# Kernel optimization log

Hardware: AMD Instinct MI355X
Metric: run time of the kernel (lower is better)

Reference implementation:

```python
import jax, jax.numpy as jnp
import numpy as np

B, T, H, V, S = 32, 1024, 512, 1024, 128
PAD = 0          # PAD_token, also the CTC blank
NEG = -1e30      # finite stand-in for -inf (grad-safe)


def setup_inputs() -> dict:
    key = jax.random.key(0)
    ks = jax.random.split(key, 5)
    padded_input = jax.random.normal(ks[0], (B, T, H), dtype=jnp.float32)
    # labels in [1, V) so no PAD inside targets -> target_lengths == S
    padded_target = jax.random.randint(ks[1], (B, S), 1, V).astype(jnp.int32)
    input_lengths = jax.random.randint(ks[2], (B,), T // 2, T + 1).astype(jnp.int32)
    W1 = jax.random.normal(ks[3], (H, H), dtype=jnp.float32) * 0.02
    b1 = jnp.zeros((H,), jnp.float32)
    W2 = jax.random.normal(ks[4], (H, V), dtype=jnp.float32) * 0.02
    b2 = jnp.zeros((V,), jnp.float32)
    return {"padded_target": padded_target, "padded_input": padded_input,
            "input_lengths": input_lengths, "W1": W1, "b1": b1, "W2": W2, "b2": b2}


def _ctc_loss(log_probs, targets, input_lengths, target_lengths, blank=PAD):
    """CTC negative log-likelihood per example (reduction='none').
    log_probs: [B,T,V] (log-softmaxed), targets: [B,S] int."""
    Bb, Tt, _ = log_probs.shape
    Ss = targets.shape[1]
    L = 2 * Ss + 1  # extended label sequence: blank,y1,blank,...,yS,blank
    ext = jnp.full((Bb, L), blank, dtype=targets.dtype).at[:, 1::2].set(targets)
    # gather log-probs of extended labels: [B,T,L] -> [T,B,L]
    lp_ext = jnp.take_along_axis(
        log_probs, jnp.broadcast_to(ext[:, None, :], (Bb, Tt, L)), axis=2)
    lp_ext = jnp.transpose(lp_ext, (1, 0, 2))
    # skip transition (s-2 -> s) allowed when ext[s] != blank and ext[s] != ext[s-2]
    skip = jnp.concatenate(
        [jnp.zeros((Bb, 2), bool),
         (ext[:, 2:] != blank) & (ext[:, 2:] != ext[:, :-2])], axis=1)

    alpha0 = jnp.full((Bb, L), NEG, jnp.float32)
    alpha0 = alpha0.at[:, 0].set(lp_ext[0, :, 0]).at[:, 1].set(lp_ext[0, :, 1])

    def step(alpha, xs):
        lp_t, t = xs
        s1 = jnp.concatenate([jnp.full((Bb, 1), NEG, jnp.float32), alpha[:, :-1]], axis=1)
        s2 = jnp.concatenate([jnp.full((Bb, 2), NEG, jnp.float32), alpha[:, :-2]], axis=1)
        a = jnp.logaddexp(alpha, s1)
        a = jnp.where(skip, jnp.logaddexp(a, s2), a)
        new = a + lp_t
        # freeze alpha past each example's input length
        new = jnp.where((t < input_lengths)[:, None], new, alpha)
        return new, None

    alpha, _ = jax.lax.scan(step, alpha0, (lp_ext[1:], jnp.arange(1, Tt)))
    end1 = jnp.take_along_axis(alpha, (2 * target_lengths - 1)[:, None], axis=1)[:, 0]
    end2 = jnp.take_along_axis(alpha, (2 * target_lengths)[:, None], axis=1)[:, 0]
    return -jnp.logaddexp(end1, end2)


def reference(padded_target, padded_input, input_lengths, W1, b1, W2, b2):
    target_lengths = jnp.sum(padded_target != PAD, axis=1).astype(jnp.int32)
    h = jnp.tanh(padded_input @ W1 + b1)          # [B,T,H]
    logits = h @ W2 + b2                           # [B,T,V]
    log_probs = jax.nn.log_softmax(logits, axis=-1)
    loss = _ctc_loss(log_probs, padded_target, input_lengths, target_lengths)
    return loss / target_lengths.astype(jnp.float32)  # [B]
```

## Files before the change

### kernel.cpp

```cpp
#include <hip/hip_runtime.h>
#include <hip/hip_bf16.h>
#include <math.h>

#define Bq 32
#define Tt 1024
#define Hh 512
#define Vv 1024
#define Ss 128

typedef short bf16x8 __attribute__((ext_vector_type(8)));
typedef float f32x4 __attribute__((ext_vector_type(4)));

#define GLDS(srcp, dstp, sz) \
  __builtin_amdgcn_global_load_lds( \
      (const __attribute__((address_space(1))) void*)(srcp), \
      (__attribute__((address_space(3))) void*)(dstp), sz, 0, 0)

__device__ __forceinline__ ushort f2bf(float v) {
  __hip_bfloat16 hv = __float2bfloat16(v);
  return *(ushort*)&hv;
}

#define BFLY_MAX(v) { \
  v = fmaxf(v, __int_as_float(__builtin_amdgcn_ds_swizzle(__float_as_int(v), 0x041F))); \
  v = fmaxf(v, __int_as_float(__builtin_amdgcn_ds_swizzle(__float_as_int(v), 0x081F))); \
  v = fmaxf(v, __int_as_float(__builtin_amdgcn_ds_swizzle(__float_as_int(v), 0x101F))); \
  v = fmaxf(v, __int_as_float(__builtin_amdgcn_ds_swizzle(__float_as_int(v), 0x201F))); }
#define BFLY_ADD(v) { \
  v += __int_as_float(__builtin_amdgcn_ds_swizzle(__float_as_int(v), 0x041F)); \
  v += __int_as_float(__builtin_amdgcn_ds_swizzle(__float_as_int(v), 0x081F)); \
  v += __int_as_float(__builtin_amdgcn_ds_swizzle(__float_as_int(v), 0x101F)); \
  v += __int_as_float(__builtin_amdgcn_ds_swizzle(__float_as_int(v), 0x201F)); }

__global__ void transpose_cvt(const float* __restrict__ in, ushort* __restrict__ out,
                              int K, int N) {
  __shared__ float tile[32][33];
  const int k0 = blockIdx.y * 32, n0 = blockIdx.x * 32;
  const int tx = threadIdx.x, ty = threadIdx.y;
  for (int i = ty; i < 32; i += 8)
    tile[i][tx] = in[(size_t)(k0 + i) * N + n0 + tx];
  __syncthreads();
  for (int i = ty; i < 32; i += 8)
    out[(size_t)(n0 + i) * K + k0 + tx] = f2bf(tile[tx][i]);
}

__global__ __launch_bounds__(256, 2)
void gemm1_fused(const float* __restrict__ A, const ushort* __restrict__ Bt,
                 const float* __restrict__ bias, ushort* __restrict__ H) {
  __shared__ ushort As[2][128 * 64];
  __shared__ ushort Bs[2][128 * 64];
  const int tid = threadIdx.x;
  const int lane = tid & 63, wave = tid >> 6;
  const int wm = wave >> 1, wn = wave & 1;
  const int q = lane >> 4, r16 = lane & 15;
  const int row0 = blockIdx.y * 128, col0 = blockIdx.x * 128;
  const int lrow = lane >> 3;
  const int swz = (lane & 7) ^ lrow;
  const int ra_ = tid >> 3;
  const int ca_ = tid & 7;
  const int ga_ = ca_ ^ (ra_ & 7);
  const int rx = r16 & 7;
  const int kx0 = (q ^ rx) * 8;
  const int kx1 = ((4 + q) ^ rx) * 8;

  float4 rA[4][2];
  auto loadA = [&](int kk) {
#pragma unroll
    for (int p = 0; p < 4; ++p) {
      const float* src = A + (size_t)(row0 + p * 32 + ra_) * Hh + kk * 64 + ga_ * 8;
      rA[p][0] = *(const float4*)(src);
      rA[p][1] = *(const float4*)(src + 4);
    }
  };
  auto storeA = [&](int d) {
#pragma unroll
    for (int p = 0; p < 4; ++p) {
      unsigned w0 = ((unsigned)f2bf(rA[p][0].y) << 16) | f2bf(rA[p][0].x);
      unsigned w1 = ((unsigned)f2bf(rA[p][0].w) << 16) | f2bf(rA[p][0].z);
      unsigned w2 = ((unsigned)f2bf(rA[p][1].y) << 16) | f2bf(rA[p][1].x);
      unsigned w3 = ((unsigned)f2bf(rA[p][1].w) << 16) | f2bf(rA[p][1].z);
      uint4 u = {w0, w1, w2, w3};
      *(uint4*)&As[d][(p * 32 + ra_) * 64 + ca_ * 8] = u;
    }
  };
  auto stageB = [&](int kk, int d) {
#pragma unroll
    for (int i = 0; i < 4; ++i) {
      const int seg = wave * 4 + i;
      const int rr = seg * 8 + lrow;
      GLDS(Bt + (size_t)(col0 + rr) * Hh + kk * 64 + swz * 8, &Bs[d][seg * 512], 16);
    }
  };

  f32x4 acc[4][4];
#pragma unroll
  for (int i = 0; i < 4; ++i)
#pragma unroll
    for (int j = 0; j < 4; ++j) acc[i][j] = (f32x4){0.f, 0.f, 0.f, 0.f};

  loadA(0);
  stageB(0, 0);
  storeA(0);
  loadA(1);
  __syncthreads();

  for (int kk = 0; kk < 8; ++kk) {
    const int d = kk & 1;
    if (kk < 7) { stageB(kk + 1, d ^ 1); storeA(d ^ 1); }
    if (kk < 6) loadA(kk + 2);
#pragma unroll
    for (int ksl = 0; ksl < 2; ++ksl) {
      const int kxo = ksl ? kx1 : kx0;
      bf16x8 af[4], bfr[4];
#pragma unroll
      for (int mi = 0; mi < 4; ++mi)
        af[mi] = *(const bf16x8*)(&As[d][((wm * 64 + mi * 16 + r16) << 6) + kxo]);
#pragma unroll
      for (int ni = 0; ni < 4; ++ni)
        bfr[ni] = *(const bf16x8*)(&Bs[d][((wn * 64 + ni * 16 + r16) << 6) + kxo]);
#pragma unroll
      for (int mi = 0; mi < 4; ++mi)
#pragma unroll
        for (int ni = 0; ni < 4; ++ni)
          acc[mi][ni] = __builtin_amdgcn_mfma_f32_16x16x32_bf16(af[mi], bfr[ni], acc[mi][ni], 0, 0, 0);
    }
    __syncthreads();
  }

#pragma unroll
  for (int ni = 0; ni < 4; ++ni) {
    const int col = col0 + wn * 64 + ni * 16 + r16;
    const float bc = bias[col];
#pragma unroll
    for (int mi = 0; mi < 4; ++mi) {
#pragma unroll
      for (int r = 0; r < 4; ++r) {
        const int row = row0 + wm * 64 + mi * 16 + q * 4 + r;
        const float v = acc[mi][ni][r] + bc;
        const float ex = __expf(2.0f * v);
        const float rc = 1.0f / (ex + 1.0f);
        H[(size_t)row * Hh + col] = f2bf((ex - 1.0f) * rc);
      }
    }
  }
}

__global__ __launch_bounds__(256, 2)
void gemm2sm(const ushort* __restrict__ Aq, const ushort* __restrict__ Bt,
             const float* __restrict__ bias, const int* __restrict__ tgt,
             ushort* __restrict__ pOdd, ushort* __restrict__ pBlank) {
  __shared__ ushort Bs[2][128 * 64];
  __shared__ float biasLds[Vv];
  __shared__ int tgLds[128];
  __shared__ float rowM[64], rowS[64], sfArr[64], blankL[64];
  __shared__ float tmpM[2][64], tmpS[2][64];

  const int tid = threadIdx.x;
  const int lane = tid & 63, wave = tid >> 6;
  const int wm = wave >> 1, wn = wave & 1;
  const int q = lane >> 4, r16 = lane & 15;
  const int row0 = blockIdx.x * 64;
  const int bEx = blockIdx.x >> 4;
  const int lrow = lane >> 3;
  const int swz = (lane & 7) ^ lrow;
  const int rx = r16 & 7;
  const int kx0 = (q ^ rx) * 8;
  const int kx1 = ((4 + q) ^ rx) * 8;

  GLDS(bias + tid * 4, (char*)biasLds + wave * 1024, 16);
  if (tid < 128) tgLds[tid] = tgt[bEx * Ss + tid];
  if (tid < 64) { rowM[tid] = -1e30f; rowS[tid] = 0.f; }

  bf16x8 af[16][2];
#pragma unroll
  for (int ks = 0; ks < 16; ++ks)
#pragma unroll
    for (int mi = 0; mi < 2; ++mi)
      af[ks][mi] = *(const bf16x8*)(Aq + (size_t)(row0 + wm * 32 + mi * 16 + r16) * Hh + ks * 32 + q * 8);

  auto stageB = [&](int nt, int kk, int d) {
#pragma unroll
    for (int i = 0; i < 4; ++i) {
      const int seg = wave * 4 + i;
      const int rr = seg * 8 + lrow;
      const int kko = kk * 64 + swz * 8;
      const ushort* src;
      if (nt < 8) src = Bt + (size_t)(nt * 128 + rr) * Hh + kko;
      else        src = Bt + (size_t)tgLds[rr] * Hh + kko;
      GLDS(src, &Bs[d][seg * 512], 16);
    }
  };

  stageB(0, 0, 0);

  f32x4 acc[2][4];
#pragma unroll
  for (int i = 0; i < 2; ++i)
#pragma unroll
    for (int j = 0; j < 4; ++j) acc[i][j] = (f32x4){0.f, 0.f, 0.f, 0.f};

  for (int nt = 0; nt < 9; ++nt) {
#pragma unroll
    for (int kk = 0; kk < 8; ++kk) {
      const int d = kk & 1;
      __syncthreads();
      if (!(nt == 8 && kk == 7)) {
        const int ntn = (kk < 7) ? nt : nt + 1;
        const int kkn = (kk < 7) ? kk + 1 : 0;
        stageB(ntn, kkn, d ^ 1);
      }
#pragma unroll
      for (int ksl = 0; ksl < 2; ++ksl) {
        const int kxo = ksl ? kx1 : kx0;
        bf16x8 bfr[4];
#pragma unroll
        for (int ni = 0; ni < 4; ++ni)
          bfr[ni] = *(const bf16x8*)(&Bs[d][((wn * 64 + ni * 16 + r16) << 6) + kxo]);
#pragma unroll
        for (int mi = 0; mi < 2; ++mi)
#pragma unroll
          for (int ni = 0; ni < 4; ++ni)
            acc[mi][ni] = __builtin_amdgcn_mfma_f32_16x16x32_bf16(af[kk * 2 + ksl][mi], bfr[ni], acc[mi][ni], 0, 0, 0);
      }
    }

    if (nt < 8) {
      float bcol[4];
#pragma unroll
      for (int ni = 0; ni < 4; ++ni) bcol[ni] = biasLds[nt * 128 + wn * 64 + ni * 16 + r16];

      float tm[2][4];
#pragma unroll
      for (int mi = 0; mi < 2; ++mi)
#pragma unroll
        for (int r = 0; r < 4; ++r) {
          float m = acc[mi][0][r] + bcol[0];
          m = fmaxf(m, acc[mi][1][r] + bcol[1]);
          m = fmaxf(m, acc[mi][2][r] + bcol[2]);
          m = fmaxf(m, acc[mi][3][r] + bcol[3]);
          BFLY_MAX(m);
          tm[mi][r] = m;
        }
      if (r16 == 0) {
#pragma unroll
        for (int mi = 0; mi < 2; ++mi) {
          float4 w = {tm[mi][0], tm[mi][1], tm[mi][2], tm[mi][3]};
          *(float4*)&tmpM[wn][wm * 32 + mi * 16 + q * 4] = w;
        }
        if (nt == 0 && wn == 0) {
#pragma unroll
          for (int mi = 0; mi < 2; ++mi) {
            float4 w = {acc[mi][0][0] + bcol[0], acc[mi][0][1] + bcol[0],
                        acc[mi][0][2] + bcol[0], acc[mi][0][3] + bcol[0]};
            *(float4*)&blankL[wm * 32 + mi * 16 + q * 4] = w;
          }
        }
      }
      __syncthreads();
      if (tid < 64) {
        const float old = rowM[tid];
        const float nm = fmaxf(old, fmaxf(tmpM[0][tid], tmpM[1][tid]));
        rowM[tid] = nm;
        sfArr[tid] = __expf(old - nm);
      }
      __syncthreads();
#pragma unroll
      for (int mi = 0; mi < 2; ++mi) {
        const float4 nm4 = *(const float4*)&rowM[wm * 32 + mi * 16 + q * 4];
#pragma unroll
        for (int r = 0; r < 4; ++r) {
          const float nm = ((const float*)&nm4)[r];
          float s = __expf(acc[mi][0][r] + bcol[0] - nm);
          s += __expf(acc[mi][1][r] + bcol[1] - nm);
          s += __expf(acc[mi][2][r] + bcol[2] - nm);
          s += __expf(acc[mi][3][r] + bcol[3] - nm);
          BFLY_ADD(s);
          tm[mi][r] = s;
        }
      }
      if (r16 == 0) {
#pragma unroll
        for (int mi = 0; mi < 2; ++mi) {
          float4 w = {tm[mi][0], tm[mi][1], tm[mi][2], tm[mi][3]};
          *(float4*)&tmpS[wn][wm * 32 + mi * 16 + q * 4] = w;
        }
      }
      __syncthreads();
      if (tid < 64)
        rowS[tid] = rowS[tid] * sfArr[tid] + tmpS[0][tid] + tmpS[1][tid];
#pragma unroll
      for (int i = 0; i < 2; ++i)
#pragma unroll
        for (int j = 0; j < 4; ++j) acc[i][j] = (f32x4){0.f, 0.f, 0.f, 0.f};
    } else {
      __syncthreads();
      if (tid < 64) {
        const float rc = rowM[tid] + __logf(rowS[tid]);
        sfArr[tid] = rc;
        pBlank[row0 + tid] = f2bf(__expf(blankL[tid] - rc) * 64.0f);
      }
      __syncthreads();
      float bcl[4];
#pragma unroll
      for (int ni = 0; ni < 4; ++ni) bcl[ni] = biasLds[tgLds[wn * 64 + ni * 16 + r16]];
#pragma unroll
      for (int mi = 0; mi < 2; ++mi) {
        const float4 rc4 = *(const float4*)&sfArr[wm * 32 + mi * 16 + q * 4];
#pragma unroll
        for (int r = 0; r < 4; ++r) {
          const float rc = ((const float*)&rc4)[r];
          const int row = row0 + wm * 32 + mi * 16 + q * 4 + r;
#pragma unroll
          for (int ni = 0; ni < 4; ++ni) {
            const float p = __expf(acc[mi][ni][r] + bcl[ni] - rc) * 64.0f;
            pOdd[(size_t)row * Ss + wn * 64 + ni * 16 + r16] = f2bf(p);
          }
        }
      }
    }
  }
}

__device__ __forceinline__ float dpp_wshr1(float x) {
  return __int_as_float(__builtin_amdgcn_update_dpp(
      0, __float_as_int(x), 0x138, 0xf, 0xf, true));
}
__device__ __forceinline__ float dpp_wave_max(float m) {
  m = fmaxf(m, __int_as_float(__builtin_amdgcn_update_dpp(0, __float_as_int(m), 0x111, 0xf, 0xf, true)));
  m = fmaxf(m, __int_as_float(__builtin_amdgcn_update_dpp(0, __float_as_int(m), 0x112, 0xf, 0xf, true)));
  m = fmaxf(m, __int_as_float(__builtin_amdgcn_update_dpp(0, __float_as_int(m), 0x114, 0xf, 0xf, true)));
  m = fmaxf(m, __int_as_float(__builtin_amdgcn_update_dpp(0, __float_as_int(m), 0x118, 0xf, 0xf, true)));
  m = fmaxf(m, __int_as_float(__builtin_amdgcn_update_dpp(__float_as_int(m), __float_as_int(m), 0x142, 0xf, 0xf, false)));
  m = fmaxf(m, __int_as_float(__builtin_amdgcn_update_dpp(__float_as_int(m), __float_as_int(m), 0x143, 0xf, 0xf, false)));
  return __int_as_float(__builtin_amdgcn_readlane(__float_as_int(m), 63));
}

__global__ __launch_bounds__(64)
void ctc_dp(const ushort* __restrict__ pOddG, const ushort* __restrict__ pBlankG,
            const int* __restrict__ tgt, const int* __restrict__ lens,
            float* __restrict__ out) {
  __shared__ ushort pO[2][72 * 128];
  __shared__ ushort pBl[2][128];
  const int b = blockIdx.x, l = threadIdx.x;
  const ushort* pObase = pOddG + (size_t)b * Tt * Ss;
  const ushort* pBbase = pBlankG + (size_t)b * Tt;
  const int* tg = tgt + b * Ss;
  const int len = lens[b];

  float sk1 = 0.f, sk3;
  if (l >= 1) sk1 = (tg[2 * l] != tg[2 * l - 1]) ? 1.f : 0.f;
  sk3 = (tg[2 * l + 1] != tg[2 * l]) ? 1.f : 0.f;

  auto stage = [&](int c, int d) {
    const ushort* src = pObase + (size_t)c * 64 * 128;
#pragma unroll
    for (int i = 0; i < 16; ++i)
      GLDS(src + (i * 64 + l) * 8, &pO[d][i * 512], 16);
    GLDS(pBbase + c * 64 + l * 2, &pBl[d][0], 4);
  };

  stage(0, 0);
  __syncthreads();

  float a0 = 0.f, a1 = 0.f, a2 = 0.f, a3 = 0.f, a4 = 0.f;
  if (l == 0) {
    a0 = __int_as_float(((unsigned)pBl[0][0]) << 16);
    a1 = __int_as_float(((unsigned)pO[0][0]) << 16);
  }
  int E = 0;

  auto renorm = [&]() {
    float m = fmaxf(fmaxf(fmaxf(a0, a1), fmaxf(a2, a3)), a4);
    const float gm = dpp_wave_max(m);
    const int e = (int)((__float_as_uint(gm) >> 23) & 255) - 127;
    int sh = 30 - e; if (sh > 120) sh = 120;
    const float scale = __uint_as_float((unsigned)(127 + sh) << 23);
    E -= sh;
    a0 *= scale; a1 *= scale; a2 *= scale; a3 *= scale; a4 *= scale;
  };

  auto run_dyn = [&](int d, int stA, int stB, int tbase) {
    const int n = stB - stA;
    if (n <= 0) return;
    unsigned qL[4], qB[4];
#pragma unroll
    for (int k = 0; k < 4; ++k) {
      const int st = stA + k;
      qL[k] = *(const unsigned*)&pO[d][(st << 7) + 2 * l];
      qB[k] = (unsigned)pBl[d][st];
    }
    auto body = [&](int i, int k) {
      const float pOa = __int_as_float(qL[k] << 16);
      const float pObv = __int_as_float(qL[k] & 0xffff0000u);
      const float pB = __int_as_float(qB[k] << 16);
      const float h3 = dpp_wshr1(a3);
      const float n0 = (a0 + h3) * pB;
      const float n1 = fmaf(sk1, h3, a1 + a0) * pOa;
      const float n2 = (a2 + a1) * pB;
      const float n3 = fmaf(sk3, a1, a3 + a2) * pObv;
      const float n4 = (a4 + a3) * pB;
      a0 = n0; a1 = n1; a2 = n2; a3 = n3; a4 = n4;
      const int st2 = stA + i + 4;
      qL[k] = *(const unsigned*)&pO[d][(st2 << 7) + 2 * l];
      qB[k] = (unsigned)pBl[d][st2];
      if (((tbase + i) & 7) == 0) renorm();
    };
    int i = 0;
    for (; i + 4 <= n; i += 4) { body(i, 0); body(i + 1, 1); body(i + 2, 2); body(i + 3, 3); }
    if ((n & 3) > 0) body(i, 0);
    if ((n & 3) > 1) body(i + 1, 1);
    if ((n & 3) > 2) body(i + 2, 2);
  };

  auto run_full = [&](int d) {
    unsigned qL[8], qB[4];
#pragma unroll
    for (int k = 0; k < 8; ++k)
      qL[k] = *(const unsigned*)&pO[d][(k << 7) + 2 * l];
#pragma unroll
    for (int j = 0; j < 4; ++j)
      qB[j] = *(const unsigned*)&pBl[d][2 * j];
    for (int i = 0; i < 64; i += 8) {
#pragma unroll
      for (int k = 0; k < 8; ++k) {
        const float pOa = __int_as_float(qL[k] << 16);
        const float pObv = __int_as_float(qL[k] & 0xffff0000u);
        const unsigned bb = qB[k >> 1];
        const float pB = __int_as_float((k & 1) ? (bb & 0xffff0000u) : (bb << 16));
        const float h3 = dpp_wshr1(a3);
        const float n0 = (a0 + h3) * pB;
        const float n1 = fmaf(sk1, h3, a1 + a0) * pOa;
        const float n2 = (a2 + a1) * pB;
        const float n3 = fmaf(sk3, a1, a3 + a2) * pObv;
        const float n4 = (a4 + a3) * pB;
        a0 = n0; a1 = n1; a2 = n2; a3 = n3; a4 = n4;
        qL[k] = *(const unsigned*)&pO[d][((i + k + 8) << 7) + 2 * l];
        if (k & 1) qB[k >> 1] = *(const unsigned*)&pBl[d][i + k + 7];
        if (k == 0) renorm();
      }
    }
  };

  if (64 < len) stage(1, 1);
  run_dyn(0, 1, (64 < len) ? 64 : len, 1);
  __syncthreads();
  const int Cfull = len >> 6;
  for (int c = 1; c < Cfull; ++c) {
    const int d = c & 1;
    if ((c + 1) * 64 < len) stage(c + 1, d ^ 1);
    run_full(d);
    __syncthreads();
  }
  if (len & 63) run_dyn(Cfull & 1, 0, len & 63, Cfull * 64);

  const int tl = __popcll(__ballot(tg[l] != 0)) + __popcll(__ballot(tg[64 + l] != 0));
  const int s1 = 2 * tl - 1, s2 = 2 * tl;
  float v = 0.f;
  const int sb = 4 * l;
  if (sb == s1 || sb == s2) v += a0;
  if (sb + 1 == s1 || sb + 1 == s2) v += a1;
  if (sb + 2 == s1 || sb + 2 == s2) v += a2;
  if (sb + 3 == s1 || sb + 3 == s2) v += a3;
  if (l == 63 && s2 == 256) v += a4;
#pragma unroll
  for (int off = 1; off < 64; off <<= 1) v += __shfl_xor(v, off);
  if (l == 0)
    out[b] = -((log2f(v) + (float)E - 6.0f * (float)len) * 0.6931471805599453f) / (float)tl;
}

extern "C" void kernel_launch(void* const* d_in, const int* in_sizes, int n_in,
                              void* d_out, int out_size, void* d_ws, size_t ws_size,
                              hipStream_t stream) {
  const int*   targets = (const int*)d_in[0];
  const float* X       = (const float*)d_in[1];
  const int*   lens    = (const int*)d_in[2];
  const float* W1      = (const float*)d_in[3];
  const float* b1      = (const float*)d_in[4];
  const float* W2      = (const float*)d_in[5];
  const float* b2      = (const float*)d_in[6];
  float* out = (float*)d_out;

  ushort* h       = (ushort*)d_ws;
  ushort* W1T     = h + (size_t)Bq * Tt * Hh;
  ushort* W2T     = W1T + (size_t)Hh * Hh;
  ushort* pOddG   = W2T + (size_t)Vv * Hh;
  ushort* pBlankG = pOddG + (size_t)Bq * Tt * Ss;

  transpose_cvt<<<dim3(Hh / 32, Hh / 32), dim3(32, 8), 0, stream>>>(W1, W1T, Hh, Hh);
  transpose_cvt<<<dim3(Vv / 32, Hh / 32), dim3(32, 8), 0, stream>>>(W2, W2T, Hh, Vv);
  gemm1_fused<<<dim3(Hh / 128, (Bq * Tt) / 128), dim3(256), 0, stream>>>(X, W1T, b1, h);
  gemm2sm<<<dim3((Bq * Tt) / 64), dim3(256), 0, stream>>>(h, W2T, b2, targets, pOddG, pBlankG);
  ctc_dp<<<dim3(Bq), dim3(64), 0, stream>>>(pOddG, pBlankG, targets, lens, out);
}
```

Before: 271.6 us.

## Restructure both GEMMs with register-resident A, triple-buffered B, and max-free softmax

gemm1 is rewritten so each block owns 64 rows of X. It converts them to bf16 once into registers and streams all four 128-column W1T tiles through a 3-stage LDS ring, using vmcnt-based waits instead of full barriers. gemm2 switches to the same 3-deep flat pipeline. Its online-softmax max tracking and per-tile barriers are replaced by a plain running sum of exp(logit), reduced once at the end. This removes per-tile cross-wave syncs, but it drops the max subtraction, so it relies on small logits to avoid overflow, and gemm1 now reloads W1T for every 64-row block.

```diff
diff --git a/kernel.cpp b/kernel.cpp
--- a/kernel.cpp
+++ b/kernel.cpp
@@ -21,11 +21,12 @@
   return *(ushort*)&hv;
 }
 
-#define BFLY_MAX(v) { \
-  v = fmaxf(v, __int_as_float(__builtin_amdgcn_ds_swizzle(__float_as_int(v), 0x041F))); \
-  v = fmaxf(v, __int_as_float(__builtin_amdgcn_ds_swizzle(__float_as_int(v), 0x081F))); \
-  v = fmaxf(v, __int_as_float(__builtin_amdgcn_ds_swizzle(__float_as_int(v), 0x101F))); \
-  v = fmaxf(v, __int_as_float(__builtin_amdgcn_ds_swizzle(__float_as_int(v), 0x201F))); }
+template <int N>
+__device__ __forceinline__ void wb() {
+  __asm__ volatile("s_waitcnt vmcnt(%0)" ::"i"(N) : "memory");
+  __builtin_amdgcn_s_barrier();
+}
+
 #define BFLY_ADD(v) { \
   v += __int_as_float(__builtin_amdgcn_ds_swizzle(__float_as_int(v), 0x041F)); \
   v += __int_as_float(__builtin_amdgcn_ds_swizzle(__float_as_int(v), 0x081F)); \
@@ -45,102 +46,94 @@
 }
 
 __global__ __launch_bounds__(256, 2)
-void gemm1_fused(const float* __restrict__ A, const ushort* __restrict__ Bt,
+void gemm1_fused(const float* __restrict__ X, const ushort* __restrict__ Bt,
                  const float* __restrict__ bias, ushort* __restrict__ H) {
-  __shared__ ushort As[2][128 * 64];
-  __shared__ ushort Bs[2][128 * 64];
+  __shared__ ushort Bs[3][128 * 64];
   const int tid = threadIdx.x;
   const int lane = tid & 63, wave = tid >> 6;
   const int wm = wave >> 1, wn = wave & 1;
   const int q = lane >> 4, r16 = lane & 15;
-  const int row0 = blockIdx.y * 128, col0 = blockIdx.x * 128;
+  const int row0 = blockIdx.x * 64;
   const int lrow = lane >> 3;
   const int swz = (lane & 7) ^ lrow;
-  const int ra_ = tid >> 3;
-  const int ca_ = tid & 7;
-  const int ga_ = ca_ ^ (ra_ & 7);
   const int rx = r16 & 7;
   const int kx0 = (q ^ rx) * 8;
   const int kx1 = ((4 + q) ^ rx) * 8;
 
-  float4 rA[4][2];
-  auto loadA = [&](int kk) {
-#pragma unroll
-    for (int p = 0; p < 4; ++p) {
-      const float* src = A + (size_t)(row0 + p * 32 + ra_) * Hh + kk * 64 + ga_ * 8;
-      rA[p][0] = *(const float4*)(src);
-      rA[p][1] = *(const float4*)(src + 4);
-    }
-  };
-  auto storeA = [&](int d) {
-#pragma unroll
-    for (int p = 0; p < 4; ++p) {
-      unsigned w0 = ((unsigned)f2bf(rA[p][0].y) << 16) | f2bf(rA[p][0].x);
-      unsigned w1 = ((unsigned)f2bf(rA[p][0].w) << 16) | f2bf(rA[p][0].z);
-      unsigned w2 = ((unsigned)f2bf(rA[p][1].y) << 16) | f2bf(rA[p][1].x);
-      unsigned w3 = ((unsigned)f2bf(rA[p][1].w) << 16) | f2bf(rA[p][1].z);
-      uint4 u = {w0, w1, w2, w3};
-      *(uint4*)&As[d][(p * 32 + ra_) * 64 + ca_ * 8] = u;
-    }
-  };
-  auto stageB = [&](int kk, int d) {
+  float bcolAll[4][4];
+#pragma unroll
+  for (int nt = 0; nt < 4; ++nt)
+#pragma unroll
+    for (int ni = 0; ni < 4; ++ni)
+      bcolAll[nt][ni] = bias[nt * 128 + wn * 64 + ni * 16 + r16];
+
+  bf16x8 af[16][2];
+#pragma unroll
+  for (int ks = 0; ks < 16; ++ks)
+#pragma unroll
+    for (int mi = 0; mi < 2; ++mi) {
+      const float* src = X + (size_t)(row0 + wm * 32 + mi * 16 + r16) * Hh + ks * 32 + q * 8;
+      const float4 f0 = *(const float4*)(src);
+      const float4 f1 = *(const float4*)(src + 4);
+      union { bf16x8 v; ushort u[8]; } pk;
+      pk.u[0] = f2bf(f0.x); pk.u[1] = f2bf(f0.y); pk.u[2] = f2bf(f0.z); pk.u[3] = f2bf(f0.w);
+      pk.u[4] = f2bf(f1.x); pk.u[5] = f2bf(f1.y); pk.u[6] = f2bf(f1.z); pk.u[7] = f2bf(f1.w);
+      af[ks][mi] = pk.v;
+    }
+
+  auto stageF = [&](int f) {
+    const int nt = f >> 3, kc = f & 7, d = f % 3;
 #pragma unroll
     for (int i = 0; i < 4; ++i) {
       const int seg = wave * 4 + i;
       const int rr = seg * 8 + lrow;
-      GLDS(Bt + (size_t)(col0 + rr) * Hh + kk * 64 + swz * 8, &Bs[d][seg * 512], 16);
-    }
-  };
-
-  f32x4 acc[4][4];
-#pragma unroll
-  for (int i = 0; i < 4; ++i)
+      GLDS(Bt + (size_t)(nt * 128 + rr) * Hh + kc * 64 + swz * 8, &Bs[d][seg * 512], 16);
+    }
+  };
+
+  stageF(0); stageF(1);
+  __syncthreads();
+
+  f32x4 acc[2][4];
+#pragma unroll
+  for (int i = 0; i < 2; ++i)
 #pragma unroll
     for (int j = 0; j < 4; ++j) acc[i][j] = (f32x4){0.f, 0.f, 0.f, 0.f};
 
-  loadA(0);
-  stageB(0, 0);
-  storeA(0);
-  loadA(1);
-  __syncthreads();
-
-  for (int kk = 0; kk < 8; ++kk) {
-    const int d = kk & 1;
-    if (kk < 7) { stageB(kk + 1, d ^ 1); storeA(d ^ 1); }
-    if (kk < 6) loadA(kk + 2);
+  for (int it = 0; it < 32; ++it) {
+    if (it < 30) { wb<4>(); stageF(it + 2); }
+    else         { wb<0>(); }
+    const int d = it % 3;
 #pragma unroll
     for (int ksl = 0; ksl < 2; ++ksl) {
       const int kxo = ksl ? kx1 : kx0;
-      bf16x8 af[4], bfr[4];
-#pragma unroll
-      for (int mi = 0; mi < 4; ++mi)
-        af[mi] = *(const bf16x8*)(&As[d][((wm * 64 + mi * 16 + r16) << 6) + kxo]);
+      bf16x8 bfr[4];
 #pragma unroll
       for (int ni = 0; ni < 4; ++ni)
         bfr[ni] = *(const bf16x8*)(&Bs[d][((wn * 64 + ni * 16 + r16) << 6) + kxo]);
-#pragma unroll
-      for (int mi = 0; mi < 4; ++mi)
+      const int kc = it & 7;
+#pragma unroll
+      for (int mi = 0; mi < 2; ++mi)
 #pragma unroll
         for (int ni = 0; ni < 4; ++ni)
-          acc[mi][ni] = __builtin_amdgcn_mfma_f32_16x16x32_bf16(af[mi], bfr[ni], acc[mi][ni], 0, 0, 0);
-    }
-    __syncthreads();
-  }
-
-#pragma unroll
-  for (int ni = 0; ni < 4; ++ni) {
-    const int col = col0 + wn * 64 + ni * 16 + r16;
-    const float bc = bias[col];
-#pragma unroll
-    for (int mi = 0; mi < 4; ++mi) {
-#pragma unroll
-      for (int r = 0; r < 4; ++r) {
-        const int row = row0 + wm * 64 + mi * 16 + q * 4 + r;
-        const float v = acc[mi][ni][r] + bc;
-        const float ex = __expf(2.0f * v);
-        const float rc = 1.0f / (ex + 1.0f);
-        H[(size_t)row * Hh + col] = f2bf((ex - 1.0f) * rc);
-      }
+          acc[mi][ni] = __builtin_amdgcn_mfma_f32_16x16x32_bf16(af[kc * 2 + ksl][mi], bfr[ni], acc[mi][ni], 0, 0, 0);
+    }
+    if ((it & 7) == 7) {
+      const int nt = it >> 3;
+#pragma unroll
+      for (int mi = 0; mi < 2; ++mi)
+#pragma unroll
+        for (int r = 0; r < 4; ++r) {
+          const int row = row0 + wm * 32 + mi * 16 + q * 4 + r;
+#pragma unroll
+          for (int ni = 0; ni < 4; ++ni) {
+            const float v = acc[mi][ni][r] + bcolAll[nt][ni];
+            const float ex = __expf(2.0f * v);
+            const float th = (ex - 1.0f) / (ex + 1.0f);
+            H[(size_t)row * Hh + nt * 128 + wn * 64 + ni * 16 + r16] = f2bf(th);
+          }
+          acc[mi][0][r] = 0.f; acc[mi][1][r] = 0.f; acc[mi][2][r] = 0.f; acc[mi][3][r] = 0.f;
+        }
     }
   }
 }
@@ -149,11 +142,12 @@
 void gemm2sm(const ushort* __restrict__ Aq, const ushort* __restrict__ Bt,
              const float* __restrict__ bias, const int* __restrict__ tgt,
              ushort* __restrict__ pOdd, ushort* __restrict__ pBlank) {
-  __shared__ ushort Bs[2][128 * 64];
+  __shared__ ushort Bs[3][128 * 64];
   __shared__ float biasLds[Vv];
   __shared__ int tgLds[128];
-  __shared__ float rowM[64], rowS[64], sfArr[64], blankL[64];
-  __shared__ float tmpM[2][64], tmpS[2][64];
+  __shared__ float blankL[64];
+  __shared__ float rowSum[64];
+  __shared__ float tmpP[2][64];
 
   const int tid = threadIdx.x;
   const int lane = tid & 63, wave = tid >> 6;
@@ -169,7 +163,6 @@
 
   GLDS(bias + tid * 4, (char*)biasLds + wave * 1024, 16);
   if (tid < 128) tgLds[tid] = tgt[bEx * Ss + tid];
-  if (tid < 64) { rowM[tid] = -1e30f; rowS[tid] = 0.f; }
 
   bf16x8 af[16][2];
 #pragma unroll
@@ -178,142 +171,113 @@
     for (int mi = 0; mi < 2; ++mi)
       af[ks][mi] = *(const bf16x8*)(Aq + (size_t)(row0 + wm * 32 + mi * 16 + r16) * Hh + ks * 32 + q * 8);
 
-  auto stageB = [&](int nt, int kk, int d) {
+  auto stageF = [&](int f) {
+    const int nt = f >> 3, kc = f & 7, d = f % 3;
 #pragma unroll
     for (int i = 0; i < 4; ++i) {
       const int seg = wave * 4 + i;
       const int rr = seg * 8 + lrow;
-      const int kko = kk * 64 + swz * 8;
       const ushort* src;
-      if (nt < 8) src = Bt + (size_t)(nt * 128 + rr) * Hh + kko;
-      else        src = Bt + (size_t)tgLds[rr] * Hh + kko;
+      if (nt < 8) src = Bt + (size_t)(nt * 128 + rr) * Hh + kc * 64 + swz * 8;
+      else        src = Bt + (size_t)tgLds[rr] * Hh + kc * 64 + swz * 8;
       GLDS(src, &Bs[d][seg * 512], 16);
     }
   };
 
-  stageB(0, 0, 0);
+  stageF(0); stageF(1);
+  __syncthreads();
 
   f32x4 acc[2][4];
 #pragma unroll
   for (int i = 0; i < 2; ++i)
 #pragma unroll
     for (int j = 0; j < 4; ++j) acc[i][j] = (f32x4){0.f, 0.f, 0.f, 0.f};
-
-  for (int nt = 0; nt < 9; ++nt) {
-#pragma unroll
-    for (int kk = 0; kk < 8; ++kk) {
-      const int d = kk & 1;
-      __syncthreads();
-      if (!(nt == 8 && kk == 7)) {
-        const int ntn = (kk < 7) ? nt : nt + 1;
-        const int kkn = (kk < 7) ? kk + 1 : 0;
-        stageB(ntn, kkn, d ^ 1);
-      }
-#pragma unroll
-      for (int ksl = 0; ksl < 2; ++ksl) {
-        const int kxo = ksl ? kx1 : kx0;
-        bf16x8 bfr[4];
+  float rowP[2][4] = {{0.f, 0.f, 0.f, 0.f}, {0.f, 0.f, 0.f, 0.f}};
+
+  for (int it = 0; it < 72; ++it) {
+    if (it < 70) { wb<4>(); stageF(it + 2); }
+    else         { wb<0>(); }
+    const int d = it % 3;
+#pragma unroll
+    for (int ksl = 0; ksl < 2; ++ksl) {
+      const int kxo = ksl ? kx1 : kx0;
+      bf16x8 bfr[4];
+#pragma unroll
+      for (int ni = 0; ni < 4; ++ni)
+        bfr[ni] = *(const bf16x8*)(&Bs[d][((wn * 64 + ni * 16 + r16) << 6) + kxo]);
+      const int kc = it & 7;
+#pragma unroll
+      for (int mi = 0; mi < 2; ++mi)
 #pragma unroll
         for (int ni = 0; ni < 4; ++ni)
-          bfr[ni] = *(const bf16x8*)(&Bs[d][((wn * 64 + ni * 16 + r16) << 6) + kxo]);
+          acc[mi][ni] = __builtin_amdgcn_mfma_f32_16x16x32_bf16(af[kc * 2 + ksl][mi], bfr[ni], acc[mi][ni], 0, 0, 0);
+    }
+
+    if ((it & 7) == 7) {
+      const int nt = it >> 3;
+      if (nt < 8) {
+        float bcol[4];
+#pragma unroll
+        for (int ni = 0; ni < 4; ++ni) bcol[ni] = biasLds[nt * 128 + wn * 64 + ni * 16 + r16];
+        if (nt == 0 && wn == 0 && r16 == 0) {
+#pragma unroll
+          for (int mi = 0; mi < 2; ++mi)
+#pragma unroll
+            for (int r = 0; r < 4; ++r)
+              blankL[wm * 32 + mi * 16 + q * 4 + r] = acc[mi][0][r] + bcol[0];
+        }
 #pragma unroll
         for (int mi = 0; mi < 2; ++mi)
 #pragma unroll
-          for (int ni = 0; ni < 4; ++ni)
-            acc[mi][ni] = __builtin_amdgcn_mfma_f32_16x16x32_bf16(af[kk * 2 + ksl][mi], bfr[ni], acc[mi][ni], 0, 0, 0);
-      }
-    }
-
-    if (nt < 8) {
-      float bcol[4];
-#pragma unroll
-      for (int ni = 0; ni < 4; ++ni) bcol[ni] = biasLds[nt * 128 + wn * 64 + ni * 16 + r16];
-
-      float tm[2][4];
-#pragma unroll
-      for (int mi = 0; mi < 2; ++mi)
-#pragma unroll
-        for (int r = 0; r < 4; ++r) {
-          float m = acc[mi][0][r] + bcol[0];
-          m = fmaxf(m, acc[mi][1][r] + bcol[1]);
-          m = fmaxf(m, acc[mi][2][r] + bcol[2]);
-          m = fmaxf(m, acc[mi][3][r] + bcol[3]);
-          BFLY_MAX(m);
-          tm[mi][r] = m;
+          for (int r = 0; r < 4; ++r) {
+            float s = __expf(acc[mi][0][r] + bcol[0]);
+            s += __expf(acc[mi][1][r] + bcol[1]);
+            s += __expf(acc[mi][2][r] + bcol[2]);
+            s += __expf(acc[mi][3][r] + bcol[3]);
+            rowP[mi][r] += s;
+            acc[mi][0][r] = 0.f; acc[mi][1][r] = 0.f; acc[mi][2][r] = 0.f; acc[mi][3][r] = 0.f;
+          }
+        if (nt == 7) {
+          float sred[2][4];
+#pragma unroll
+          for (int mi = 0; mi < 2; ++mi)
+#pragma unroll
+            for (int r = 0; r < 4; ++r) {
+              float s = rowP[mi][r];
+              BFLY_ADD(s);
+              sred[mi][r] = s;
+            }
+          if (r16 == 0) {
+#pragma unroll
+            for (int mi = 0; mi < 2; ++mi) {
+              float4 w = {sred[mi][0], sred[mi][1], sred[mi][2], sred[mi][3]};
+              *(float4*)&tmpP[wn][wm * 32 + mi * 16 + q * 4] = w;
+            }
+          }
+          __syncthreads();
+          if (tid < 64) {
+            const float tot = tmpP[0][tid] + tmpP[1][tid];
+            rowSum[tid] = tot;
+            pBlank[row0 + tid] = f2bf(__expf(blankL[tid]) * 64.0f / tot);
+          }
+          __syncthreads();
         }
-      if (r16 == 0) {
+      } else {
+        float bcl[4];
+#pragma unroll
+        for (int ni = 0; ni < 4; ++ni) bcl[ni] = biasLds[tgLds[wn * 64 + ni * 16 + r16]];
 #pragma unroll
         for (int mi = 0; mi < 2; ++mi) {
-          float4 w = {tm[mi][0], tm[mi][1], tm[mi][2], tm[mi][3]};
-          *(float4*)&tmpM[wn][wm * 32 + mi * 16 + q * 4] = w;
-        }
-        if (nt == 0 && wn == 0) {
-#pragma unroll
-          for (int mi = 0; mi < 2; ++mi) {
-            float4 w = {acc[mi][0][0] + bcol[0], acc[mi][0][1] + bcol[0],
-                        acc[mi][0][2] + bcol[0], acc[mi][0][3] + bcol[0]};
-            *(float4*)&blankL[wm * 32 + mi * 16 + q * 4] = w;
-          }
-        }
-      }
-      __syncthreads();
-      if (tid < 64) {
-        const float old = rowM[tid];
-        const float nm = fmaxf(old, fmaxf(tmpM[0][tid], tmpM[1][tid]));
-        rowM[tid] = nm;
-        sfArr[tid] = __expf(old - nm);
-      }
-      __syncthreads();
-#pragma unroll
-      for (int mi = 0; mi < 2; ++mi) {
-        const float4 nm4 = *(const float4*)&rowM[wm * 32 + mi * 16 + q * 4];
-#pragma unroll
-        for (int r = 0; r < 4; ++r) {
-          const float nm = ((const float*)&nm4)[r];
-          float s = __expf(acc[mi][0][r] + bcol[0] - nm);
-          s += __expf(acc[mi][1][r] + bcol[1] - nm);
-          s += __expf(acc[mi][2][r] + bcol[2] - nm);
-          s += __expf(acc[mi][3][r] + bcol[3] - nm);
-          BFLY_ADD(s);
-          tm[mi][r] = s;
-        }
-      }
-      if (r16 == 0) {
-#pragma unroll
-        for (int mi = 0; mi < 2; ++mi) {
-          float4 w = {tm[mi][0], tm[mi][1], tm[mi][2], tm[mi][3]};
-          *(float4*)&tmpS[wn][wm * 32 + mi * 16 + q * 4] = w;
-        }
-      }
-      __syncthreads();
-      if (tid < 64)
-        rowS[tid] = rowS[tid] * sfArr[tid] + tmpS[0][tid] + tmpS[1][tid];
-#pragma unroll
-      for (int i = 0; i < 2; ++i)
-#pragma unroll
-        for (int j = 0; j < 4; ++j) acc[i][j] = (f32x4){0.f, 0.f, 0.f, 0.f};
-    } else {
-      __syncthreads();
-      if (tid < 64) {
-        const float rc = rowM[tid] + __logf(rowS[tid]);
-        sfArr[tid] = rc;
-        pBlank[row0 + tid] = f2bf(__expf(blankL[tid] - rc) * 64.0f);
-      }
-      __syncthreads();
-      float bcl[4];
-#pragma unroll
-      for (int ni = 0; ni < 4; ++ni) bcl[ni] = biasLds[tgLds[wn * 64 + ni * 16 + r16]];
-#pragma unroll
-      for (int mi = 0; mi < 2; ++mi) {
-        const float4 rc4 = *(const float4*)&sfArr[wm * 32 + mi * 16 + q * 4];
-#pragma unroll
-        for (int r = 0; r < 4; ++r) {
-          const float rc = ((const float*)&rc4)[r];
-          const int row = row0 + wm * 32 + mi * 16 + q * 4 + r;
-#pragma unroll
-          for (int ni = 0; ni < 4; ++ni) {
-            const float p = __expf(acc[mi][ni][r] + bcl[ni] - rc) * 64.0f;
-            pOdd[(size_t)row * Ss + wn * 64 + ni * 16 + r16] = f2bf(p);
+          const float4 rs4 = *(const float4*)&rowSum[wm * 32 + mi * 16 + q * 4];
+#pragma unroll
+          for (int r = 0; r < 4; ++r) {
+            const float sc = 64.0f / ((const float*)&rs4)[r];
+            const int row = row0 + wm * 32 + mi * 16 + q * 4 + r;
+#pragma unroll
+            for (int ni = 0; ni < 4; ++ni) {
+              const float p = __expf(acc[mi][ni][r] + bcl[ni]) * sc;
+              pOdd[(size_t)row * Ss + wn * 64 + ni * 16 + r16] = f2bf(p);
+            }
           }
         }
       }
@@ -488,7 +452,7 @@
 
   transpose_cvt<<<dim3(Hh / 32, Hh / 32), dim3(32, 8), 0, stream>>>(W1, W1T, Hh, Hh);
   transpose_cvt<<<dim3(Vv / 32, Hh / 32), dim3(32, 8), 0, stream>>>(W2, W2T, Hh, Vv);
-  gemm1_fused<<<dim3(Hh / 128, (Bq * Tt) / 128), dim3(256), 0, stream>>>(X, W1T, b1, h);
+  gemm1_fused<<<dim3((Bq * Tt) / 64), dim3(256), 0, stream>>>(X, W1T, b1, h);
   gemm2sm<<<dim3((Bq * Tt) / 64), dim3(256), 0, stream>>>(h, W2T, b2, targets, pOddG, pBlankG);
   ctc_dp<<<dim3(Bq), dim3(64), 0, stream>>>(pOddG, pBlankG, targets, lens, out);
 }
```

Result: slower. 362.9 us (+33.6%).
